# Kernel tuning notes

Hardware: AMD Instinct MI355X
Metric: run time of the kernel (lower is better)

## Reference

```python
import jax, jax.numpy as jnp
import numpy as np

RADIUS = 0.5
K = 32
EPS = 1e-5


def ball_query(pc, new_pc, radius, k):
    """pc [B,3,N], new_pc [B,3,S] -> idx [B,S,k] int32, num [B,S] int32.
    First k in-radius points per query; empty slots filled with the first
    found index (standard ball-query semantics of QueryDepthPoint)."""
    d2 = jnp.sum((new_pc[:, :, :, None] - pc[:, :, None, :]) ** 2, axis=1)  # [B,S,N]
    B, S, N = d2.shape
    mask = d2 < radius * radius
    rank = jnp.cumsum(mask.astype(jnp.int32), axis=-1) - 1          # rank among valid
    slot = jnp.where(mask & (rank < k), rank, k)                     # k = dummy slot
    jidx = jnp.broadcast_to(jnp.arange(N, dtype=jnp.int32), (B, S, N))
    bidx = jnp.arange(B)[:, None, None]
    sidx = jnp.arange(S)[None, :, None]
    idx = jnp.zeros((B, S, k + 1), jnp.int32).at[bidx, sidx, slot].set(jidx)
    idx = idx[..., :k]
    num = jnp.sum(mask, axis=-1).astype(jnp.int32)                   # [B,S]
    nvalid = jnp.minimum(num, k)
    idx = jnp.where(jnp.arange(k) < nvalid[..., None], idx, idx[..., :1])
    return idx, num


def conv_bn_relu(x, w, b, g, be):
    """1x1 Conv2d + BatchNorm2d (batch stats, training mode) + ReLU.
    x [B,Cin,S,K], w [Cout,Cin]."""
    y = jnp.einsum('bcsk,oc->bosk', x, w) + b[None, :, None, None]
    mean = jnp.mean(y, axis=(0, 2, 3), keepdims=True)
    var = jnp.var(y, axis=(0, 2, 3), keepdims=True)
    y = (y - mean) * jax.lax.rsqrt(var + EPS) * g[None, :, None, None] + be[None, :, None, None]
    return jax.nn.relu(y)


def setup_inputs() -> dict:
    key = jax.random.key(0)
    ks = jax.random.split(key, 8)
    B, N, S, C = 4, 8192, 2048, 16
    mlp = [32, 32, 64]
    cin = C + 3  # use_xyz concat
    pc = jax.random.normal(ks[0], (B, 3, N), jnp.float32)
    feat = jax.random.normal(ks[1], (B, C, N), jnp.float32)
    new_pc = jax.random.normal(ks[2], (B, 3, S), jnp.float32)
    def kaiming(k, co, ci):
        return jax.random.normal(k, (co, ci), jnp.float32) * np.sqrt(2.0 / ci)
    w1 = kaiming(ks[3], mlp[0], cin)
    w2 = kaiming(ks[4], mlp[1], mlp[0])
    w3 = kaiming(ks[5], mlp[2], mlp[1])
    return {
        'pc': pc, 'feat': feat, 'new_pc': new_pc,
        'w1': w1, 'b1': jnp.zeros((mlp[0],)), 'g1': jnp.ones((mlp[0],)), 'be1': jnp.zeros((mlp[0],)),
        'w2': w2, 'b2': jnp.zeros((mlp[1],)), 'g2': jnp.ones((mlp[1],)), 'be2': jnp.zeros((mlp[1],)),
        'w3': w3, 'b3': jnp.zeros((mlp[2],)), 'g3': jnp.ones((mlp[2],)), 'be3': jnp.zeros((mlp[2],)),
    }


def reference(pc, feat, new_pc, w1, b1, g1, be1, w2, b2, g2, be2, w3, b3, g3, be3):
    B = pc.shape[0]
    S = new_pc.shape[2]
    idx, num = ball_query(pc, new_pc, RADIUS, K)          # [B,S,K], [B,S]
    bidx = jnp.arange(B)[:, None, None]
    # gather neighbors: fancy index -> [B,S,K,3] / [B,S,K,Cf], then to channel-first
    grouped_pc = pc[bidx, :, idx].transpose(0, 3, 1, 2)   # [B,3,S,K]
    grouped_pc = grouped_pc - new_pc[:, :, :, None]       # center on query
    grouped_feat = feat[bidx, :, idx].transpose(0, 3, 1, 2)  # [B,Cf,S,K]
    x = jnp.concatenate([grouped_pc, grouped_feat], axis=1)  # [B,Cf+3,S,K]
    x = conv_bn_relu(x, w1, b1, g1, be1)
    x = conv_bn_relu(x, w2, b2, g2, be2)
    x = conv_bn_relu(x, w3, b3, g3, be3)
    valid = (num > 0).astype(x.dtype)[:, None, :, None]   # [B,1,S,1]
    return x * valid
```

## Files before the change

### kernel.cpp

```cpp
#include <hip/hip_runtime.h>

#define BQ_RADIUS2 0.25f
#define KK 32
#define NB 4
#define NP 8192
#define NS 2048
#define C1 32
#define C2 32
#define C3 64
#define EPSBN 1e-5f
#define RTOT 65536
#define MTOT (NB*NS*KK)
#define NSLOT 32

#define OFF_G     0
#define OFF_IDX   655360
#define OFF_VALID 917504
#define OFF_P1    925696
#define OFF_P2    927744
#define OFF_P3    929792
#define OFF_PAR1  933888
#define OFF_PAR2  933952
#define OFF_PAR3  934016

__global__ __launch_bounds__(256) void k_pack(const float* __restrict__ pc,
                                              const float* __restrict__ feat,
                                              float* __restrict__ g,
                                              float* __restrict__ partials) {
  const int t = blockIdx.x * 256 + threadIdx.x;
  if (t < 8192) partials[t] = 0.f;
  const int b = t >> 13;
  const int j = t & (NP - 1);
  const float* pcb = pc + b * 3 * NP;
  float* gp = g + (size_t)t * 20;
  gp[0] = pcb[j];
  gp[1] = pcb[NP + j];
  gp[2] = pcb[2 * NP + j];
  const float* fb = feat + b * 16 * NP;
#pragma unroll
  for (int c = 0; c < 16; c++) gp[3 + c] = fb[c * NP + j];
  gp[19] = 0.f;
}

__global__ __launch_bounds__(256) void k_ballquery(const float* __restrict__ pc,
                                                   const float* __restrict__ newpc,
                                                   int* __restrict__ idx,
                                                   int* __restrict__ valid) {
  __shared__ int buf[4][KK];
  const int tid = threadIdx.x;
  const int w = tid >> 6, lane = tid & 63;
  const int gq = blockIdx.x * 4 + w;
  const int b = gq >> 11, s = gq & (NS - 1);
  const float* np0 = newpc + b * 3 * NS;
  const float qx = np0[s], qy = np0[NS + s], qz = np0[2 * NS + s];
  const float* px = pc + b * 3 * NP;
  const float* py = px + NP;
  const float* pz = px + 2 * NP;
  if (lane == 0) buf[w][0] = 0;
  int cnt = 0;
  for (int j0 = 0; j0 < NP; j0 += 256) {
    const int jb = j0 + lane * 4;
    const float4 vx = *(const float4*)(px + jb);
    const float4 vy = *(const float4*)(py + jb);
    const float4 vz = *(const float4*)(pz + jb);
    int mm = 0;
    {
      float dx = __fsub_rn(qx, vx.x), dy = __fsub_rn(qy, vy.x), dz = __fsub_rn(qz, vz.x);
      if (__fadd_rn(__fadd_rn(__fmul_rn(dx, dx), __fmul_rn(dy, dy)), __fmul_rn(dz, dz)) < BQ_RADIUS2) mm |= 1;
    }
    {
      float dx = __fsub_rn(qx, vx.y), dy = __fsub_rn(qy, vy.y), dz = __fsub_rn(qz, vz.y);
      if (__fadd_rn(__fadd_rn(__fmul_rn(dx, dx), __fmul_rn(dy, dy)), __fmul_rn(dz, dz)) < BQ_RADIUS2) mm |= 2;
    }
    {
      float dx = __fsub_rn(qx, vx.z), dy = __fsub_rn(qy, vy.z), dz = __fsub_rn(qz, vz.z);
      if (__fadd_rn(__fadd_rn(__fmul_rn(dx, dx), __fmul_rn(dy, dy)), __fmul_rn(dz, dz)) < BQ_RADIUS2) mm |= 4;
    }
    {
      float dx = __fsub_rn(qx, vx.w), dy = __fsub_rn(qy, vy.w), dz = __fsub_rn(qz, vz.w);
      if (__fadd_rn(__fadd_rn(__fmul_rn(dx, dx), __fmul_rn(dy, dy)), __fmul_rn(dz, dz)) < BQ_RADIUS2) mm |= 8;
    }
    const int c4 = __popc(mm);
    int pre = c4;
#pragma unroll
    for (int off = 1; off < 64; off <<= 1) {
      int v = __shfl_up(pre, off);
      if (lane >= off) pre += v;
    }
    const int total = __shfl(pre, 63);
    if (mm) {
      int base = cnt + pre - c4;
#pragma unroll
      for (int i = 0; i < 4; i++) {
        if ((mm >> i) & 1) {
          if (base < KK) buf[w][base] = jb + i;
          base++;
        }
      }
    }
    cnt += total;
    if (cnt >= KK) break;
  }
  __syncthreads();
  if (lane < KK) {
    const int f = cnt < KK ? cnt : KK;
    const int i0 = buf[w][0];
    idx[gq * KK + lane] = (lane < f) ? buf[w][lane] : i0;
  }
  if (lane == 0) valid[gq] = (cnt > 0);
}

__global__ __launch_bounds__(256) void k_conv1(const float* __restrict__ g,
                                               const int* __restrict__ idx,
                                               const float* __restrict__ newpc,
                                               const float* __restrict__ w1,
                                               const float* __restrict__ b1,
                                               float* __restrict__ y,
                                               float* __restrict__ partial) {
  __shared__ float wl[C1 * 20];
  __shared__ float bl[C1];
  __shared__ float red[16][2 * C1 + 1];
  const int tid = threadIdx.x;
  for (int i = tid; i < C1 * 20; i += 256) {
    const int o = i / 20, c = i - o * 20;
    wl[i] = (c < 19) ? w1[o * 19 + c] : 0.f;
  }
  if (tid < C1) bl[tid] = b1[tid];
  __syncthreads();
  const int pos = blockIdx.x * 256 + tid;
  const int b = pos >> 16;
  const int r = pos & (RTOT - 1);
  const int s = r >> 5;
  const int j = idx[pos];
  const float4* gp = (const float4*)(g + (size_t)(b * NP + j) * 20);
  const float4 v0 = gp[0], v1 = gp[1], v2 = gp[2], v3 = gp[3], v4 = gp[4];
  const float* np0 = newpc + b * 3 * NS;
  float xr[20];
  xr[0] = v0.x - np0[s]; xr[1] = v0.y - np0[NS + s]; xr[2] = v0.z - np0[2 * NS + s]; xr[3] = v0.w;
  xr[4] = v1.x; xr[5] = v1.y; xr[6] = v1.z; xr[7] = v1.w;
  xr[8] = v2.x; xr[9] = v2.y; xr[10] = v2.z; xr[11] = v2.w;
  xr[12] = v3.x; xr[13] = v3.y; xr[14] = v3.z; xr[15] = v3.w;
  xr[16] = v4.x; xr[17] = v4.y; xr[18] = v4.z; xr[19] = v4.w;
  float* yb = y + ((size_t)b * C3) * RTOT + r;
  const int grp = tid >> 4;
  const bool lead = (tid & 15) == 0;
#pragma unroll
  for (int o = 0; o < C1; o++) {
    float acc = bl[o];
    const float4* wr = (const float4*)&wl[o * 20];
#pragma unroll
    for (int ct = 0; ct < 5; ct++) {
      const float4 wv = wr[ct];
      acc = fmaf(wv.x, xr[4 * ct + 0], acc);
      acc = fmaf(wv.y, xr[4 * ct + 1], acc);
      acc = fmaf(wv.z, xr[4 * ct + 2], acc);
      acc = fmaf(wv.w, xr[4 * ct + 3], acc);
    }
    yb[(size_t)o * RTOT] = acc;
    float a = acc, q = acc * acc;
    a += __shfl_xor(a, 1); q += __shfl_xor(q, 1);
    a += __shfl_xor(a, 2); q += __shfl_xor(q, 2);
    a += __shfl_xor(a, 4); q += __shfl_xor(q, 4);
    a += __shfl_xor(a, 8); q += __shfl_xor(q, 8);
    if (lead) { red[grp][o] = a; red[grp][C1 + o] = q; }
  }
  __syncthreads();
  if (tid < 2 * C1) {
    float v = 0.f;
#pragma unroll
    for (int gq = 0; gq < 16; gq++) v += red[gq][tid];
    atomicAdd(&partial[(blockIdx.x & (NSLOT - 1)) * 2 * C1 + tid], v);
  }
}

__global__ __launch_bounds__(256) void k_conv2(const float* __restrict__ w2,
                                               const float* __restrict__ b2,
                                               const float* __restrict__ par,
                                               float* y,
                                               float* __restrict__ partial) {
  __shared__ float wl[C2 * C1];
  __shared__ float bl[C2];
  __shared__ float pl[2 * C1];
  __shared__ float red[16][2 * C2 + 1];
  const int tid = threadIdx.x;
  for (int i = tid; i < C2 * C1; i += 256) wl[i] = w2[i];
  if (tid < C2) bl[tid] = b2[tid];
  if (tid < 2 * C1) pl[tid] = par[tid];
  __syncthreads();
  const int pos = blockIdx.x * 256 + tid;
  const int b = pos >> 16;
  const int r = pos & (RTOT - 1);
  float* yb = y + ((size_t)b * C3) * RTOT + r;
  float xr[C1];
#pragma unroll
  for (int c = 0; c < C1; c++) {
    const float v = yb[(size_t)c * RTOT];
    xr[c] = fmaxf(fmaf(v, pl[c], pl[C1 + c]), 0.f);
  }
  const int grp = tid >> 4;
  const bool lead = (tid & 15) == 0;
#pragma unroll
  for (int o = 0; o < C2; o++) {
    float acc = bl[o];
    const float4* wr = (const float4*)&wl[o * C1];
#pragma unroll
    for (int ct = 0; ct < C1 / 4; ct++) {
      const float4 wv = wr[ct];
      acc = fmaf(wv.x, xr[4 * ct + 0], acc);
      acc = fmaf(wv.y, xr[4 * ct + 1], acc);
      acc = fmaf(wv.z, xr[4 * ct + 2], acc);
      acc = fmaf(wv.w, xr[4 * ct + 3], acc);
    }
    yb[(size_t)o * RTOT] = acc;
    float a = acc, q = acc * acc;
    a += __shfl_xor(a, 1); q += __shfl_xor(q, 1);
    a += __shfl_xor(a, 2); q += __shfl_xor(q, 2);
    a += __shfl_xor(a, 4); q += __shfl_xor(q, 4);
    a += __shfl_xor(a, 8); q += __shfl_xor(q, 8);
    if (lead) { red[grp][o] = a; red[grp][C2 + o] = q; }
  }
  __syncthreads();
  if (tid < 2 * C2) {
    float v = 0.f;
#pragma unroll
    for (int gq = 0; gq < 16; gq++) v += red[gq][tid];
    atomicAdd(&partial[(blockIdx.x & (NSLOT - 1)) * 2 * C2 + tid], v);
  }
}

__global__ __launch_bounds__(256) void k_conv3(const float* __restrict__ w3,
                                               const float* __restrict__ b3,
                                               const float* __restrict__ par,
                                               float* y,
                                               float* __restrict__ partial) {
  __shared__ float wl[C3 * C2];
  __shared__ float bl[C3];
  __shared__ float pl[2 * C2];
  __shared__ float red[16][2 * C3 + 1];
  const int tid = threadIdx.x;
  for (int i = tid; i < C3 * C2; i += 256) wl[i] = w3[i];
  if (tid < C3) bl[tid] = b3[tid];
  if (tid < 2 * C2) pl[tid] = par[tid];
  __syncthreads();
  const int pos = blockIdx.x * 256 + tid;
  const int b = pos >> 16;
  const int r = pos & (RTOT - 1);
  float* yb = y + ((size_t)b * C3) * RTOT + r;
  float xr[C2];
#pragma unroll
  for (int c = 0; c < C2; c++) {
    const float v = yb[(size_t)c * RTOT];
    xr[c] = fmaxf(fmaf(v, pl[c], pl[C2 + c]), 0.f);
  }
  const int grp = tid >> 4;
  const bool lead = (tid & 15) == 0;
#pragma unroll
  for (int o = 0; o < C3; o++) {
    float acc = bl[o];
    const float4* wr = (const float4*)&wl[o * C2];
#pragma unroll
    for (int ct = 0; ct < C2 / 4; ct++) {
      const float4 wv = wr[ct];
      acc = fmaf(wv.x, xr[4 * ct + 0], acc);
      acc = fmaf(wv.y, xr[4 * ct + 1], acc);
      acc = fmaf(wv.z, xr[4 * ct + 2], acc);
      acc = fmaf(wv.w, xr[4 * ct + 3], acc);
    }
    yb[(size_t)o * RTOT] = acc;
    float a = acc, q = acc * acc;
    a += __shfl_xor(a, 1); q += __shfl_xor(q, 1);
    a += __shfl_xor(a, 2); q += __shfl_xor(q, 2);
    a += __shfl_xor(a, 4); q += __shfl_xor(q, 4);
    a += __shfl_xor(a, 8); q += __shfl_xor(q, 8);
    if (lead) { red[grp][o] = a; red[grp][C3 + o] = q; }
  }
  __syncthreads();
  if (tid < 2 * C3) {
    float v = 0.f;
#pragma unroll
    for (int gq = 0; gq < 16; gq++) v += red[gq][tid];
    atomicAdd(&partial[(blockIdx.x & (NSLOT - 1)) * 2 * C3 + tid], v);
  }
}

__global__ void k_params(const float* __restrict__ partial,
                         const float* __restrict__ gamma,
                         const float* __restrict__ beta,
                         float* __restrict__ params, int C) {
  __shared__ float tot[2 * C3];
  const int t = threadIdx.x;
  float v = 0.f;
#pragma unroll 1
  for (int sl = 0; sl < NSLOT; ++sl) v += partial[sl * 2 * C + t];
  tot[t] = v;
  __syncthreads();
  if (t < C) {
    const float inv = 1.0f / (float)MTOT;
    const float mean = tot[t] * inv;
    const float ex2 = tot[C + t] * inv;
    const float var = ex2 - mean * mean;
    const float sc = gamma[t] * rsqrtf(var + EPSBN);
    params[t] = sc;
    params[C + t] = beta[t] - mean * sc;
  }
}

__global__ __launch_bounds__(256) void k_final(float* __restrict__ out,
                                               const float* __restrict__ par,
                                               const int* __restrict__ valid) {
  const int t = blockIdx.x * 256 + threadIdx.x;
  const size_t e = (size_t)t * 4;
  const int b = t >> 20;
  const int o = (t >> 14) & 63;
  const int s = (t & 16383) >> 3;
  const float sc = par[o], sh = par[C3 + o];
  const float m = valid[(b << 11) + s] ? 1.f : 0.f;
  float4 v = *(float4*)(out + e);
  v.x = fmaxf(fmaf(v.x, sc, sh), 0.f) * m;
  v.y = fmaxf(fmaf(v.y, sc, sh), 0.f) * m;
  v.z = fmaxf(fmaf(v.z, sc, sh), 0.f) * m;
  v.w = fmaxf(fmaf(v.w, sc, sh), 0.f) * m;
  *(float4*)(out + e) = v;
}

extern "C" void kernel_launch(void* const* d_in, const int* in_sizes, int n_in,
                              void* d_out, int out_size, void* d_ws, size_t ws_size,
                              hipStream_t stream) {
  const float* pc    = (const float*)d_in[0];
  const float* feat  = (const float*)d_in[1];
  const float* newpc = (const float*)d_in[2];
  const float* w1 = (const float*)d_in[3];
  const float* b1 = (const float*)d_in[4];
  const float* g1 = (const float*)d_in[5];
  const float* be1 = (const float*)d_in[6];
  const float* w2 = (const float*)d_in[7];
  const float* b2 = (const float*)d_in[8];
  const float* g2 = (const float*)d_in[9];
  const float* be2 = (const float*)d_in[10];
  const float* w3 = (const float*)d_in[11];
  const float* b3 = (const float*)d_in[12];
  const float* g3 = (const float*)d_in[13];
  const float* be3 = (const float*)d_in[14];

  float* ws = (float*)d_ws;
  float* gbuf  = ws + OFF_G;
  int*   idx   = (int*)(ws + OFF_IDX);
  int*   valid = (int*)(ws + OFF_VALID);
  float* p1 = ws + OFF_P1;
  float* p2 = ws + OFF_P2;
  float* p3 = ws + OFF_P3;
  float* par1 = ws + OFF_PAR1;
  float* par2 = ws + OFF_PAR2;
  float* par3 = ws + OFF_PAR3;
  float* out = (float*)d_out;

  k_pack<<<dim3(128), dim3(256), 0, stream>>>(pc, feat, gbuf, p1);
  k_ballquery<<<dim3(2048), dim3(256), 0, stream>>>(pc, newpc, idx, valid);
  k_conv1<<<dim3(1024), dim3(256), 0, stream>>>(gbuf, idx, newpc, w1, b1, out, p1);
  k_params<<<dim3(1), dim3(2 * C1), 0, stream>>>(p1, g1, be1, par1, C1);
  k_conv2<<<dim3(1024), dim3(256), 0, stream>>>(w2, b2, par1, out, p2);
  k_params<<<dim3(1), dim3(2 * C2), 0, stream>>>(p2, g2, be2, par2, C2);
  k_conv3<<<dim3(1024), dim3(256), 0, stream>>>(w3, b3, par2, out, p3);
  k_params<<<dim3(1), dim3(2 * C3), 0, stream>>>(p3, g3, be3, par3, C3);
  k_final<<<dim3(16384), dim3(256), 0, stream>>>(out, par3, valid);
}
```

Measured before the change: 277.5 us.

## Process four positions per thread in conv kernels with float4 loads and stores

Each thread in the three conv kernels now handles four consecutive positions. Each weight read from LDS is reused across four outputs, and activations move as float4 vector loads and stores. The grids shrink from 1024 to 256 blocks, which on a 256-CU part means about one block per CU, and launch bounds of (256,1) allow much higher register use. The trade-off is lower occupancy for hiding gather and global-memory latency, plus large float4 register arrays that risk spilling.

```diff
diff --git a/kernel.cpp b/kernel.cpp
--- a/kernel.cpp
+++ b/kernel.cpp
@@ -110,13 +110,13 @@
   if (lane == 0) valid[gq] = (cnt > 0);
 }
 
-__global__ __launch_bounds__(256) void k_conv1(const float* __restrict__ g,
-                                               const int* __restrict__ idx,
-                                               const float* __restrict__ newpc,
-                                               const float* __restrict__ w1,
-                                               const float* __restrict__ b1,
-                                               float* __restrict__ y,
-                                               float* __restrict__ partial) {
+__global__ __launch_bounds__(256, 1) void k_conv1(const float* __restrict__ g,
+                                                  const int* __restrict__ idx,
+                                                  const float* __restrict__ newpc,
+                                                  const float* __restrict__ w1,
+                                                  const float* __restrict__ b1,
+                                                  float* __restrict__ y,
+                                                  float* __restrict__ partial) {
   __shared__ float wl[C1 * 20];
   __shared__ float bl[C1];
   __shared__ float red[16][2 * C1 + 1];
@@ -128,36 +128,48 @@
   if (tid < C1) bl[tid] = b1[tid];
   __syncthreads();
   const int pos = blockIdx.x * 256 + tid;
-  const int b = pos >> 16;
-  const int r = pos & (RTOT - 1);
+  const int p4 = pos << 2;
+  const int b = p4 >> 16;
+  const int r = p4 & (RTOT - 1);
   const int s = r >> 5;
-  const int j = idx[pos];
-  const float4* gp = (const float4*)(g + (size_t)(b * NP + j) * 20);
-  const float4 v0 = gp[0], v1 = gp[1], v2 = gp[2], v3 = gp[3], v4 = gp[4];
+  const int4 jj = *(const int4*)(idx + p4);
   const float* np0 = newpc + b * 3 * NS;
-  float xr[20];
-  xr[0] = v0.x - np0[s]; xr[1] = v0.y - np0[NS + s]; xr[2] = v0.z - np0[2 * NS + s]; xr[3] = v0.w;
-  xr[4] = v1.x; xr[5] = v1.y; xr[6] = v1.z; xr[7] = v1.w;
-  xr[8] = v2.x; xr[9] = v2.y; xr[10] = v2.z; xr[11] = v2.w;
-  xr[12] = v3.x; xr[13] = v3.y; xr[14] = v3.z; xr[15] = v3.w;
-  xr[16] = v4.x; xr[17] = v4.y; xr[18] = v4.z; xr[19] = v4.w;
+  const float nx = np0[s], ny = np0[NS + s], nz = np0[2 * NS + s];
+  float4 xr[20];
+#define LOADPT(COMP, J) { \
+    const float4* gp = (const float4*)(g + (size_t)(b * NP + (J)) * 20); \
+    const float4 a0 = gp[0], a1 = gp[1], a2 = gp[2], a3 = gp[3], a4 = gp[4]; \
+    xr[0].COMP = a0.x - nx; xr[1].COMP = a0.y - ny; xr[2].COMP = a0.z - nz; xr[3].COMP = a0.w; \
+    xr[4].COMP = a1.x; xr[5].COMP = a1.y; xr[6].COMP = a1.z; xr[7].COMP = a1.w; \
+    xr[8].COMP = a2.x; xr[9].COMP = a2.y; xr[10].COMP = a2.z; xr[11].COMP = a2.w; \
+    xr[12].COMP = a3.x; xr[13].COMP = a3.y; xr[14].COMP = a3.z; xr[15].COMP = a3.w; \
+    xr[16].COMP = a4.x; xr[17].COMP = a4.y; xr[18].COMP = a4.z; xr[19].COMP = a4.w; }
+  LOADPT(x, jj.x) LOADPT(y, jj.y) LOADPT(z, jj.z) LOADPT(w, jj.w)
+#undef LOADPT
   float* yb = y + ((size_t)b * C3) * RTOT + r;
   const int grp = tid >> 4;
   const bool lead = (tid & 15) == 0;
-#pragma unroll
+#pragma unroll 4
   for (int o = 0; o < C1; o++) {
-    float acc = bl[o];
+    const float bo = bl[o];
+    float4 acc = make_float4(bo, bo, bo, bo);
     const float4* wr = (const float4*)&wl[o * 20];
 #pragma unroll
     for (int ct = 0; ct < 5; ct++) {
       const float4 wv = wr[ct];
-      acc = fmaf(wv.x, xr[4 * ct + 0], acc);
-      acc = fmaf(wv.y, xr[4 * ct + 1], acc);
-      acc = fmaf(wv.z, xr[4 * ct + 2], acc);
-      acc = fmaf(wv.w, xr[4 * ct + 3], acc);
-    }
-    yb[(size_t)o * RTOT] = acc;
-    float a = acc, q = acc * acc;
+      const float4 x0 = xr[4 * ct + 0], x1 = xr[4 * ct + 1], x2 = xr[4 * ct + 2], x3 = xr[4 * ct + 3];
+      acc.x = fmaf(wv.x, x0.x, acc.x); acc.y = fmaf(wv.x, x0.y, acc.y);
+      acc.z = fmaf(wv.x, x0.z, acc.z); acc.w = fmaf(wv.x, x0.w, acc.w);
+      acc.x = fmaf(wv.y, x1.x, acc.x); acc.y = fmaf(wv.y, x1.y, acc.y);
+      acc.z = fmaf(wv.y, x1.z, acc.z); acc.w = fmaf(wv.y, x1.w, acc.w);
+      acc.x = fmaf(wv.z, x2.x, acc.x); acc.y = fmaf(wv.z, x2.y, acc.y);
+      acc.z = fmaf(wv.z, x2.z, acc.z); acc.w = fmaf(wv.z, x2.w, acc.w);
+      acc.x = fmaf(wv.w, x3.x, acc.x); acc.y = fmaf(wv.w, x3.y, acc.y);
+      acc.z = fmaf(wv.w, x3.z, acc.z); acc.w = fmaf(wv.w, x3.w, acc.w);
+    }
+    *(float4*)(yb + (size_t)o * RTOT) = acc;
+    float a = (acc.x + acc.y) + (acc.z + acc.w);
+    float q = (acc.x * acc.x + acc.y * acc.y) + (acc.z * acc.z + acc.w * acc.w);
     a += __shfl_xor(a, 1); q += __shfl_xor(q, 1);
     a += __shfl_xor(a, 2); q += __shfl_xor(q, 2);
     a += __shfl_xor(a, 4); q += __shfl_xor(q, 4);
@@ -173,11 +185,11 @@
   }
 }
 
-__global__ __launch_bounds__(256) void k_conv2(const float* __restrict__ w2,
-                                               const float* __restrict__ b2,
-                                               const float* __restrict__ par,
-                                               float* y,
-                                               float* __restrict__ partial) {
+__global__ __launch_bounds__(256, 1) void k_conv2(const float* __restrict__ w2,
+                                                  const float* __restrict__ b2,
+                                                  const float* __restrict__ par,
+                                                  float* y,
+                                                  float* __restrict__ partial) {
   __shared__ float wl[C2 * C1];
   __shared__ float bl[C2];
   __shared__ float pl[2 * C1];
@@ -188,31 +200,44 @@
   if (tid < 2 * C1) pl[tid] = par[tid];
   __syncthreads();
   const int pos = blockIdx.x * 256 + tid;
-  const int b = pos >> 16;
-  const int r = pos & (RTOT - 1);
+  const int p4 = pos << 2;
+  const int b = p4 >> 16;
+  const int r = p4 & (RTOT - 1);
   float* yb = y + ((size_t)b * C3) * RTOT + r;
-  float xr[C1];
+  float4 xr[C1];
 #pragma unroll
   for (int c = 0; c < C1; c++) {
-    const float v = yb[(size_t)c * RTOT];
-    xr[c] = fmaxf(fmaf(v, pl[c], pl[C1 + c]), 0.f);
+    float4 v = *(const float4*)(yb + (size_t)c * RTOT);
+    const float sc = pl[c], sh = pl[C1 + c];
+    v.x = fmaxf(fmaf(v.x, sc, sh), 0.f);
+    v.y = fmaxf(fmaf(v.y, sc, sh), 0.f);
+    v.z = fmaxf(fmaf(v.z, sc, sh), 0.f);
+    v.w = fmaxf(fmaf(v.w, sc, sh), 0.f);
+    xr[c] = v;
   }
   const int grp = tid >> 4;
   const bool lead = (tid & 15) == 0;
-#pragma unroll
+#pragma unroll 4
   for (int o = 0; o < C2; o++) {
-    float acc = bl[o];
+    const float bo = bl[o];
+    float4 acc = make_float4(bo, bo, bo, bo);
     const float4* wr = (const float4*)&wl[o * C1];
 #pragma unroll
     for (int ct = 0; ct < C1 / 4; ct++) {
       const float4 wv = wr[ct];
-      acc = fmaf(wv.x, xr[4 * ct + 0], acc);
-      acc = fmaf(wv.y, xr[4 * ct + 1], acc);
-      acc = fmaf(wv.z, xr[4 * ct + 2], acc);
-      acc = fmaf(wv.w, xr[4 * ct + 3], acc);
-    }
-    yb[(size_t)o * RTOT] = acc;
-    float a = acc, q = acc * acc;
+      const float4 x0 = xr[4 * ct + 0], x1 = xr[4 * ct + 1], x2 = xr[4 * ct + 2], x3 = xr[4 * ct + 3];
+      acc.x = fmaf(wv.x, x0.x, acc.x); acc.y = fmaf(wv.x, x0.y, acc.y);
+      acc.z = fmaf(wv.x, x0.z, acc.z); acc.w = fmaf(wv.x, x0.w, acc.w);
+      acc.x = fmaf(wv.y, x1.x, acc.x); acc.y = fmaf(wv.y, x1.y, acc.y);
+      acc.z = fmaf(wv.y, x1.z, acc.z); acc.w = fmaf(wv.y, x1.w, acc.w);
+      acc.x = fmaf(wv.z, x2.x, acc.x); acc.y = fmaf(wv.z, x2.y, acc.y);
+      acc.z = fmaf(wv.z, x2.z, acc.z); acc.w = fmaf(wv.z, x2.w, acc.w);
+      acc.x = fmaf(wv.w, x3.x, acc.x); acc.y = fmaf(wv.w, x3.y, acc.y);
+      acc.z = fmaf(wv.w, x3.z, acc.z); acc.w = fmaf(wv.w, x3.w, acc.w);
+    }
+    *(float4*)(yb + (size_t)o * RTOT) = acc;
+    float a = (acc.x + acc.y) + (acc.z + acc.w);
+    float q = (acc.x * acc.x + acc.y * acc.y) + (acc.z * acc.z + acc.w * acc.w);
     a += __shfl_xor(a, 1); q += __shfl_xor(q, 1);
     a += __shfl_xor(a, 2); q += __shfl_xor(q, 2);
     a += __shfl_xor(a, 4); q += __shfl_xor(q, 4);
@@ -228,11 +253,11 @@
   }
 }
 
-__global__ __launch_bounds__(256) void k_conv3(const float* __restrict__ w3,
-                                               const float* __restrict__ b3,
-                                               const float* __restrict__ par,
-                                               float* y,
-                                               float* __restrict__ partial) {
+__global__ __launch_bounds__(256, 1) void k_conv3(const float* __restrict__ w3,
+                                                  const float* __restrict__ b3,
+                                                  const float* __restrict__ par,
+                                                  float* y,
+                                                  float* __restrict__ partial) {
   __shared__ float wl[C3 * C2];
   __shared__ float bl[C3];
   __shared__ float pl[2 * C2];
@@ -243,31 +268,44 @@
   if (tid < 2 * C2) pl[tid] = par[tid];
   __syncthreads();
   const int pos = blockIdx.x * 256 + tid;
-  const int b = pos >> 16;
-  const int r = pos & (RTOT - 1);
+  const int p4 = pos << 2;
+  const int b = p4 >> 16;
+  const int r = p4 & (RTOT - 1);
   float* yb = y + ((size_t)b * C3) * RTOT + r;
-  float xr[C2];
+  float4 xr[C2];
 #pragma unroll
   for (int c = 0; c < C2; c++) {
-    const float v = yb[(size_t)c * RTOT];
-    xr[c] = fmaxf(fmaf(v, pl[c], pl[C2 + c]), 0.f);
+    float4 v = *(const float4*)(yb + (size_t)c * RTOT);
+    const float sc = pl[c], sh = pl[C2 + c];
+    v.x = fmaxf(fmaf(v.x, sc, sh), 0.f);
+    v.y = fmaxf(fmaf(v.y, sc, sh), 0.f);
+    v.z = fmaxf(fmaf(v.z, sc, sh), 0.f);
+    v.w = fmaxf(fmaf(v.w, sc, sh), 0.f);
+    xr[c] = v;
   }
   const int grp = tid >> 4;
   const bool lead = (tid & 15) == 0;
-#pragma unroll
+#pragma unroll 4
   for (int o = 0; o < C3; o++) {
-    float acc = bl[o];
+    const float bo = bl[o];
+    float4 acc = make_float4(bo, bo, bo, bo);
     const float4* wr = (const float4*)&wl[o * C2];
 #pragma unroll
     for (int ct = 0; ct < C2 / 4; ct++) {
       const float4 wv = wr[ct];
-      acc = fmaf(wv.x, xr[4 * ct + 0], acc);
-      acc = fmaf(wv.y, xr[4 * ct + 1], acc);
-      acc = fmaf(wv.z, xr[4 * ct + 2], acc);
-      acc = fmaf(wv.w, xr[4 * ct + 3], acc);
-    }
-    yb[(size_t)o * RTOT] = acc;
-    float a = acc, q = acc * acc;
+      const float4 x0 = xr[4 * ct + 0], x1 = xr[4 * ct + 1], x2 = xr[4 * ct + 2], x3 = xr[4 * ct + 3];
+      acc.x = fmaf(wv.x, x0.x, acc.x); acc.y = fmaf(wv.x, x0.y, acc.y);
+      acc.z = fmaf(wv.x, x0.z, acc.z); acc.w = fmaf(wv.x, x0.w, acc.w);
+      acc.x = fmaf(wv.y, x1.x, acc.x); acc.y = fmaf(wv.y, x1.y, acc.y);
+      acc.z = fmaf(wv.y, x1.z, acc.z); acc.w = fmaf(wv.y, x1.w, acc.w);
+      acc.x = fmaf(wv.z, x2.x, acc.x); acc.y = fmaf(wv.z, x2.y, acc.y);
+      acc.z = fmaf(wv.z, x2.z, acc.z); acc.w = fmaf(wv.z, x2.w, acc.w);
+      acc.x = fmaf(wv.w, x3.x, acc.x); acc.y = fmaf(wv.w, x3.y, acc.y);
+      acc.z = fmaf(wv.w, x3.z, acc.z); acc.w = fmaf(wv.w, x3.w, acc.w);
+    }
+    *(float4*)(yb + (size_t)o * RTOT) = acc;
+    float a = (acc.x + acc.y) + (acc.z + acc.w);
+    float q = (acc.x * acc.x + acc.y * acc.y) + (acc.z * acc.z + acc.w * acc.w);
     a += __shfl_xor(a, 1); q += __shfl_xor(q, 1);
     a += __shfl_xor(a, 2); q += __shfl_xor(q, 2);
     a += __shfl_xor(a, 4); q += __shfl_xor(q, 4);
@@ -356,11 +394,11 @@
 
   k_pack<<<dim3(128), dim3(256), 0, stream>>>(pc, feat, gbuf, p1);
   k_ballquery<<<dim3(2048), dim3(256), 0, stream>>>(pc, newpc, idx, valid);
-  k_conv1<<<dim3(1024), dim3(256), 0, stream>>>(gbuf, idx, newpc, w1, b1, out, p1);
+  k_conv1<<<dim3(256), dim3(256), 0, stream>>>(gbuf, idx, newpc, w1, b1, out, p1);
   k_params<<<dim3(1), dim3(2 * C1), 0, stream>>>(p1, g1, be1, par1, C1);
-  k_conv2<<<dim3(1024), dim3(256), 0, stream>>>(w2, b2, par1, out, p2);
+  k_conv2<<<dim3(256), dim3(256), 0, stream>>>(w2, b2, par1, out, p2);
   k_params<<<dim3(1), dim3(2 * C2), 0, stream>>>(p2, g2, be2, par2, C2);
-  k_conv3<<<dim3(1024), dim3(256), 0, stream>>>(w3, b3, par2, out, p3);
+  k_conv3<<<dim3(256), dim3(256), 0, stream>>>(w3, b3, par2, out, p3);
   k_params<<<dim3(1), dim3(2 * C3), 0, stream>>>(p3, g3, be3, par3, C3);
   k_final<<<dim3(16384), dim3(256), 0, stream>>>(out, par3, valid);
 }
```

After: 245.5 us. 11.5% less time.

## Recompute conv3 instead of storing it, fuse final BN/ReLU/mask, widen conv2/3 per thread

Applied to the files above, without the earlier changes.

Conv3 is split into a stats-only pass that never writes its 64-channel output and a second pass that recomputes conv3 and applies the final BN, ReLU and validity mask directly. This removes the separate final elementwise kernel and one full write-then-read of the largest activation. Conv2 writes into channels 32..63 so conv3 can read its input while overwriting channels 0..63 in the final pass. Conv2 and conv3 now process two positions per thread with float2 accesses, weights are read from global/scalar memory instead of LDS, and blocks shrink to 128 threads. The cost is redoing the conv3 matmul and rereading conv2 output twice.

```diff
diff --git a/kernel.cpp b/kernel.cpp
--- a/kernel.cpp
+++ b/kernel.cpp
@@ -110,52 +110,38 @@
   if (lane == 0) valid[gq] = (cnt > 0);
 }
 
-__global__ __launch_bounds__(256) void k_conv1(const float* __restrict__ g,
+__global__ __launch_bounds__(128) void k_conv1(const float* __restrict__ g,
                                                const int* __restrict__ idx,
                                                const float* __restrict__ newpc,
                                                const float* __restrict__ w1,
                                                const float* __restrict__ b1,
                                                float* __restrict__ y,
                                                float* __restrict__ partial) {
-  __shared__ float wl[C1 * 20];
-  __shared__ float bl[C1];
-  __shared__ float red[16][2 * C1 + 1];
-  const int tid = threadIdx.x;
-  for (int i = tid; i < C1 * 20; i += 256) {
-    const int o = i / 20, c = i - o * 20;
-    wl[i] = (c < 19) ? w1[o * 19 + c] : 0.f;
-  }
-  if (tid < C1) bl[tid] = b1[tid];
-  __syncthreads();
-  const int pos = blockIdx.x * 256 + tid;
+  __shared__ float red[8][2 * C1 + 1];
+  const int tid = threadIdx.x;
+  const int pos = blockIdx.x * 128 + tid;
   const int b = pos >> 16;
   const int r = pos & (RTOT - 1);
   const int s = r >> 5;
   const int j = idx[pos];
   const float4* gp = (const float4*)(g + (size_t)(b * NP + j) * 20);
-  const float4 v0 = gp[0], v1 = gp[1], v2 = gp[2], v3 = gp[3], v4 = gp[4];
+  const float4 a0 = gp[0], a1 = gp[1], a2 = gp[2], a3 = gp[3], a4 = gp[4];
   const float* np0 = newpc + b * 3 * NS;
   float xr[20];
-  xr[0] = v0.x - np0[s]; xr[1] = v0.y - np0[NS + s]; xr[2] = v0.z - np0[2 * NS + s]; xr[3] = v0.w;
-  xr[4] = v1.x; xr[5] = v1.y; xr[6] = v1.z; xr[7] = v1.w;
-  xr[8] = v2.x; xr[9] = v2.y; xr[10] = v2.z; xr[11] = v2.w;
-  xr[12] = v3.x; xr[13] = v3.y; xr[14] = v3.z; xr[15] = v3.w;
-  xr[16] = v4.x; xr[17] = v4.y; xr[18] = v4.z; xr[19] = v4.w;
+  xr[0] = a0.x - np0[s]; xr[1] = a0.y - np0[NS + s]; xr[2] = a0.z - np0[2 * NS + s]; xr[3] = a0.w;
+  xr[4] = a1.x; xr[5] = a1.y; xr[6] = a1.z; xr[7] = a1.w;
+  xr[8] = a2.x; xr[9] = a2.y; xr[10] = a2.z; xr[11] = a2.w;
+  xr[12] = a3.x; xr[13] = a3.y; xr[14] = a3.z; xr[15] = a3.w;
+  xr[16] = a4.x; xr[17] = a4.y; xr[18] = a4.z; xr[19] = a4.w;
   float* yb = y + ((size_t)b * C3) * RTOT + r;
   const int grp = tid >> 4;
   const bool lead = (tid & 15) == 0;
-#pragma unroll
+#pragma unroll 4
   for (int o = 0; o < C1; o++) {
-    float acc = bl[o];
-    const float4* wr = (const float4*)&wl[o * 20];
-#pragma unroll
-    for (int ct = 0; ct < 5; ct++) {
-      const float4 wv = wr[ct];
-      acc = fmaf(wv.x, xr[4 * ct + 0], acc);
-      acc = fmaf(wv.y, xr[4 * ct + 1], acc);
-      acc = fmaf(wv.z, xr[4 * ct + 2], acc);
-      acc = fmaf(wv.w, xr[4 * ct + 3], acc);
-    }
+    float acc = b1[o];
+    const float* wr = w1 + o * 19;
+#pragma unroll
+    for (int c = 0; c < 19; c++) acc = fmaf(wr[c], xr[c], acc);
     yb[(size_t)o * RTOT] = acc;
     float a = acc, q = acc * acc;
     a += __shfl_xor(a, 1); q += __shfl_xor(q, 1);
@@ -168,51 +154,52 @@
   if (tid < 2 * C1) {
     float v = 0.f;
 #pragma unroll
-    for (int gq = 0; gq < 16; gq++) v += red[gq][tid];
+    for (int gq = 0; gq < 8; gq++) v += red[gq][tid];
     atomicAdd(&partial[(blockIdx.x & (NSLOT - 1)) * 2 * C1 + tid], v);
   }
 }
 
-__global__ __launch_bounds__(256) void k_conv2(const float* __restrict__ w2,
+__global__ __launch_bounds__(128) void k_conv2(const float* __restrict__ w2,
                                                const float* __restrict__ b2,
                                                const float* __restrict__ par,
-                                               float* y,
+                                               float* __restrict__ y,
                                                float* __restrict__ partial) {
-  __shared__ float wl[C2 * C1];
-  __shared__ float bl[C2];
-  __shared__ float pl[2 * C1];
-  __shared__ float red[16][2 * C2 + 1];
-  const int tid = threadIdx.x;
-  for (int i = tid; i < C2 * C1; i += 256) wl[i] = w2[i];
-  if (tid < C2) bl[tid] = b2[tid];
-  if (tid < 2 * C1) pl[tid] = par[tid];
-  __syncthreads();
-  const int pos = blockIdx.x * 256 + tid;
-  const int b = pos >> 16;
-  const int r = pos & (RTOT - 1);
-  float* yb = y + ((size_t)b * C3) * RTOT + r;
-  float xr[C1];
+  __shared__ float red[8][2 * C2 + 1];
+  const int tid = threadIdx.x;
+  const int pos = blockIdx.x * 128 + tid;
+  const int p2 = pos << 1;
+  const int b = p2 >> 16;
+  const int r = p2 & (RTOT - 1);
+  const float* xb = y + ((size_t)b * C3) * RTOT + r;
+  float* yb = y + ((size_t)(b * C3 + C1)) * RTOT + r;
+  float2 xr[C1];
 #pragma unroll
   for (int c = 0; c < C1; c++) {
-    const float v = yb[(size_t)c * RTOT];
-    xr[c] = fmaxf(fmaf(v, pl[c], pl[C1 + c]), 0.f);
+    float2 v = *(const float2*)(xb + (size_t)c * RTOT);
+    const float sc = par[c], sh = par[C1 + c];
+    v.x = fmaxf(fmaf(v.x, sc, sh), 0.f);
+    v.y = fmaxf(fmaf(v.y, sc, sh), 0.f);
+    xr[c] = v;
   }
   const int grp = tid >> 4;
   const bool lead = (tid & 15) == 0;
-#pragma unroll
+#pragma unroll 4
   for (int o = 0; o < C2; o++) {
-    float acc = bl[o];
-    const float4* wr = (const float4*)&wl[o * C1];
+    const float bo = b2[o];
+    float2 acc = make_float2(bo, bo);
+    const float4* wr = (const float4*)(w2 + o * C1);
 #pragma unroll
     for (int ct = 0; ct < C1 / 4; ct++) {
       const float4 wv = wr[ct];
-      acc = fmaf(wv.x, xr[4 * ct + 0], acc);
-      acc = fmaf(wv.y, xr[4 * ct + 1], acc);
-      acc = fmaf(wv.z, xr[4 * ct + 2], acc);
-      acc = fmaf(wv.w, xr[4 * ct + 3], acc);
-    }
-    yb[(size_t)o * RTOT] = acc;
-    float a = acc, q = acc * acc;
+      const float2 x0 = xr[4 * ct + 0], x1 = xr[4 * ct + 1], x2 = xr[4 * ct + 2], x3 = xr[4 * ct + 3];
+      acc.x = fmaf(wv.x, x0.x, acc.x); acc.y = fmaf(wv.x, x0.y, acc.y);
+      acc.x = fmaf(wv.y, x1.x, acc.x); acc.y = fmaf(wv.y, x1.y, acc.y);
+      acc.x = fmaf(wv.z, x2.x, acc.x); acc.y = fmaf(wv.z, x2.y, acc.y);
+      acc.x = fmaf(wv.w, x3.x, acc.x); acc.y = fmaf(wv.w, x3.y, acc.y);
+    }
+    *(float2*)(yb + (size_t)o * RTOT) = acc;
+    float a = acc.x + acc.y;
+    float q = fmaf(acc.x, acc.x, acc.y * acc.y);
     a += __shfl_xor(a, 1); q += __shfl_xor(q, 1);
     a += __shfl_xor(a, 2); q += __shfl_xor(q, 2);
     a += __shfl_xor(a, 4); q += __shfl_xor(q, 4);
@@ -223,41 +210,88 @@
   if (tid < 2 * C2) {
     float v = 0.f;
 #pragma unroll
-    for (int gq = 0; gq < 16; gq++) v += red[gq][tid];
+    for (int gq = 0; gq < 8; gq++) v += red[gq][tid];
     atomicAdd(&partial[(blockIdx.x & (NSLOT - 1)) * 2 * C2 + tid], v);
   }
 }
 
-__global__ __launch_bounds__(256) void k_conv3(const float* __restrict__ w3,
-                                               const float* __restrict__ b3,
-                                               const float* __restrict__ par,
-                                               float* y,
-                                               float* __restrict__ partial) {
-  __shared__ float wl[C3 * C2];
-  __shared__ float bl[C3];
-  __shared__ float pl[2 * C2];
-  __shared__ float red[16][2 * C3 + 1];
-  const int tid = threadIdx.x;
-  for (int i = tid; i < C3 * C2; i += 256) wl[i] = w3[i];
-  if (tid < C3) bl[tid] = b3[tid];
-  if (tid < 2 * C2) pl[tid] = par[tid];
-  __syncthreads();
-  const int pos = blockIdx.x * 256 + tid;
+__global__ __launch_bounds__(128) void k_conv3s(const float* __restrict__ w3,
+                                                const float* __restrict__ b3,
+                                                const float* __restrict__ par,
+                                                const float* __restrict__ y,
+                                                float* __restrict__ partial) {
+  __shared__ float red[8][2 * C3 + 1];
+  const int tid = threadIdx.x;
+  const int pos = blockIdx.x * 128 + tid;
+  const int p2 = pos << 1;
+  const int b = p2 >> 16;
+  const int r = p2 & (RTOT - 1);
+  const float* xb = y + ((size_t)(b * C3 + C1)) * RTOT + r;
+  float2 xr[C2];
+#pragma unroll
+  for (int c = 0; c < C2; c++) {
+    float2 v = *(const float2*)(xb + (size_t)c * RTOT);
+    const float sc = par[c], sh = par[C2 + c];
+    v.x = fmaxf(fmaf(v.x, sc, sh), 0.f);
+    v.y = fmaxf(fmaf(v.y, sc, sh), 0.f);
+    xr[c] = v;
+  }
+  const int grp = tid >> 4;
+  const bool lead = (tid & 15) == 0;
+#pragma unroll 4
+  for (int o = 0; o < C3; o++) {
+    const float bo = b3[o];
+    float2 acc = make_float2(bo, bo);
+    const float4* wr = (const float4*)(w3 + o * C2);
+#pragma unroll
+    for (int ct = 0; ct < C2 / 4; ct++) {
+      const float4 wv = wr[ct];
+      const float2 x0 = xr[4 * ct + 0], x1 = xr[4 * ct + 1], x2 = xr[4 * ct + 2], x3 = xr[4 * ct + 3];
+      acc.x = fmaf(wv.x, x0.x, acc.x); acc.y = fmaf(wv.x, x0.y, acc.y);
+      acc.x = fmaf(wv.y, x1.x, acc.x); acc.y = fmaf(wv.y, x1.y, acc.y);
+      acc.x = fmaf(wv.z, x2.x, acc.x); acc.y = fmaf(wv.z, x2.y, acc.y);
+      acc.x = fmaf(wv.w, x3.x, acc.x); acc.y = fmaf(wv.w, x3.y, acc.y);
+    }
+    float a = acc.x + acc.y;
+    float q = fmaf(acc.x, acc.x, acc.y * acc.y);
+    a += __shfl_xor(a, 1); q += __shfl_xor(q, 1);
+    a += __shfl_xor(a, 2); q += __shfl_xor(q, 2);
+    a += __shfl_xor(a, 4); q += __shfl_xor(q, 4);
+    a += __shfl_xor(a, 8); q += __shfl_xor(q, 8);
+    if (lead) { red[grp][o] = a; red[grp][C3 + o] = q; }
+  }
+  __syncthreads();
+  {
+    float v = 0.f;
+#pragma unroll
+    for (int gq = 0; gq < 8; gq++) v += red[gq][tid];
+    atomicAdd(&partial[(blockIdx.x & (NSLOT - 1)) * 2 * C3 + tid], v);
+  }
+}
+
+__global__ __launch_bounds__(128) void k_conv3f(const float* __restrict__ w3,
+                                                const float* __restrict__ b3,
+                                                const float* __restrict__ par2,
+                                                const float* __restrict__ par3,
+                                                const int* __restrict__ valid,
+                                                float* __restrict__ y) {
+  const int tid = threadIdx.x;
+  const int pos = blockIdx.x * 128 + tid;
   const int b = pos >> 16;
   const int r = pos & (RTOT - 1);
+  const float* xb = y + ((size_t)(b * C3 + C1)) * RTOT + r;
+  float xr[C2];
+#pragma unroll
+  for (int c = 0; c < C2; c++) {
+    const float v = xb[(size_t)c * RTOT];
+    xr[c] = fmaxf(fmaf(v, par2[c], par2[C2 + c]), 0.f);
+  }
+  const float m = valid[(b << 11) + (r >> 5)] ? 1.f : 0.f;
   float* yb = y + ((size_t)b * C3) * RTOT + r;
-  float xr[C2];
-#pragma unroll
-  for (int c = 0; c < C2; c++) {
-    const float v = yb[(size_t)c * RTOT];
-    xr[c] = fmaxf(fmaf(v, pl[c], pl[C2 + c]), 0.f);
-  }
-  const int grp = tid >> 4;
-  const bool lead = (tid & 15) == 0;
-#pragma unroll
+#pragma unroll 4
   for (int o = 0; o < C3; o++) {
-    float acc = bl[o];
-    const float4* wr = (const float4*)&wl[o * C2];
+    float acc = b3[o];
+    const float4* wr = (const float4*)(w3 + o * C2);
 #pragma unroll
     for (int ct = 0; ct < C2 / 4; ct++) {
       const float4 wv = wr[ct];
@@ -266,20 +300,7 @@
       acc = fmaf(wv.z, xr[4 * ct + 2], acc);
       acc = fmaf(wv.w, xr[4 * ct + 3], acc);
     }
-    yb[(size_t)o * RTOT] = acc;
-    float a = acc, q = acc * acc;
-    a += __shfl_xor(a, 1); q += __shfl_xor(q, 1);
-    a += __shfl_xor(a, 2); q += __shfl_xor(q, 2);
-    a += __shfl_xor(a, 4); q += __shfl_xor(q, 4);
-    a += __shfl_xor(a, 8); q += __shfl_xor(q, 8);
-    if (lead) { red[grp][o] = a; red[grp][C3 + o] = q; }
-  }
-  __syncthreads();
-  if (tid < 2 * C3) {
-    float v = 0.f;
-#pragma unroll
-    for (int gq = 0; gq < 16; gq++) v += red[gq][tid];
-    atomicAdd(&partial[(blockIdx.x & (NSLOT - 1)) * 2 * C3 + tid], v);
+    yb[(size_t)o * RTOT] = fmaxf(fmaf(acc, par3[o], par3[C3 + o]), 0.f) * m;
   }
 }
 
@@ -303,24 +324,6 @@
     params[t] = sc;
     params[C + t] = beta[t] - mean * sc;
   }
-}
-
-__global__ __launch_bounds__(256) void k_final(float* __restrict__ out,
-                                               const float* __restrict__ par,
-                                               const int* __restrict__ valid) {
-  const int t = blockIdx.x * 256 + threadIdx.x;
-  const size_t e = (size_t)t * 4;
-  const int b = t >> 20;
-  const int o = (t >> 14) & 63;
-  const int s = (t & 16383) >> 3;
-  const float sc = par[o], sh = par[C3 + o];
-  const float m = valid[(b << 11) + s] ? 1.f : 0.f;
-  float4 v = *(float4*)(out + e);
-  v.x = fmaxf(fmaf(v.x, sc, sh), 0.f) * m;
-  v.y = fmaxf(fmaf(v.y, sc, sh), 0.f) * m;
-  v.z = fmaxf(fmaf(v.z, sc, sh), 0.f) * m;
-  v.w = fmaxf(fmaf(v.w, sc, sh), 0.f) * m;
-  *(float4*)(out + e) = v;
 }
 
 extern "C" void kernel_launch(void* const* d_in, const int* in_sizes, int n_in,
@@ -356,11 +359,11 @@
 
   k_pack<<<dim3(128), dim3(256), 0, stream>>>(pc, feat, gbuf, p1);
   k_ballquery<<<dim3(2048), dim3(256), 0, stream>>>(pc, newpc, idx, valid);
-  k_conv1<<<dim3(1024), dim3(256), 0, stream>>>(gbuf, idx, newpc, w1, b1, out, p1);
+  k_conv1<<<dim3(2048), dim3(128), 0, stream>>>(gbuf, idx, newpc, w1, b1, out, p1);
   k_params<<<dim3(1), dim3(2 * C1), 0, stream>>>(p1, g1, be1, par1, C1);
-  k_conv2<<<dim3(1024), dim3(256), 0, stream>>>(w2, b2, par1, out, p2);
+  k_conv2<<<dim3(1024), dim3(128), 0, stream>>>(w2, b2, par1, out, p2);
   k_params<<<dim3(1), dim3(2 * C2), 0, stream>>>(p2, g2, be2, par2, C2);
-  k_conv3<<<dim3(1024), dim3(256), 0, stream>>>(w3, b3, par2, out, p3);
+  k_conv3s<<<dim3(1024), dim3(128), 0, stream>>>(w3, b3, par2, out, p3);
   k_params<<<dim3(1), dim3(2 * C3), 0, stream>>>(p3, g3, be3, par3, C3);
-  k_final<<<dim3(16384), dim3(256), 0, stream>>>(out, par3, valid);
-}
+  k_conv3f<<<dim3(2048), dim3(128), 0, stream>>>(w3, b3, par2, par3, valid, out);
+}
```

Result: slower. 298.3 us (+7.5%).
